# Performance work log

Hardware: AMD Instinct MI355X
Metric: run time of the kernel (lower is better)

The kernel has to match this reference:

```python
import jax, jax.numpy as jnp
import numpy as np

B, T, C = 2, 2048, 1024
NH = 16
HS = C // NH            # 64
BD = max(HS // 4, 16)   # 16
HORIZON = 32


def _windows(t, delta):
    # t: [B, nh, T, d] -> [B, nh, T, delta, d]; window w at pos i maps to original index i-delta+1+w
    padded = jnp.pad(t, ((0, 0), (0, 0), (delta - 1, 0), (0, 0)))
    idx = jnp.arange(t.shape[2])[:, None] + jnp.arange(delta)[None, :]
    return padded[:, :, idx]


def setup_inputs() -> dict:
    key = jax.random.key(0)
    ks = jax.random.split(key, 16)
    s = 0.02
    inp = {
        "x": jax.random.normal(ks[0], (B, T, C), dtype=jnp.float32),
        # weights stored [in, out] (transposed vs torch Linear)
        "w_disp": jax.random.normal(ks[1], (C, NH * BD), dtype=jnp.float32) * s,
        "b_disp": jnp.zeros((NH * BD,), dtype=jnp.float32),
        "w_val": jax.random.normal(ks[2], (C, C), dtype=jnp.float32) * s,
        "b_val": jnp.zeros((C,), dtype=jnp.float32),
        "rel_pos_emb": jax.random.normal(ks[3], (HORIZON, BD), dtype=jnp.float32) * s,
        "w_state": jax.random.normal(ks[4], (BD, BD), dtype=jnp.float32) * s,
        "b_state": jnp.zeros((BD,), dtype=jnp.float32),
        "w_strain": jax.random.normal(ks[5], (BD, BD), dtype=jnp.float32) * s,
        "b_strain": jnp.zeros((BD,), dtype=jnp.float32),
        "w_state_i": jax.random.normal(ks[6], (BD, BD), dtype=jnp.float32) * s,
        "w_state_j": jax.random.normal(ks[7], (BD, BD), dtype=jnp.float32) * s,
        "w_pos": jax.random.normal(ks[8], (BD, BD), dtype=jnp.float32) * s,
        "w_bond_out": jax.random.normal(ks[9], (BD, 1), dtype=jnp.float32) * s,
        "b_bond_out": jnp.zeros((1,), dtype=jnp.float32),
        "w_damage": jax.random.normal(ks[10], (BD, BD), dtype=jnp.float32) * s,
        "b_damage": jnp.zeros((BD,), dtype=jnp.float32),
        "w_damage_out": jax.random.normal(ks[11], (BD, 1), dtype=jnp.float32) * s,
        "b_damage_out": jnp.full((1,), -3.0, dtype=jnp.float32),
        "w_cproj": jax.random.normal(ks[12], (C, C), dtype=jnp.float32) * s,
        "b_cproj": jnp.zeros((C,), dtype=jnp.float32),
    }
    return inp


def reference(x, w_disp, b_disp, w_val, b_val, rel_pos_emb, w_state, b_state,
              w_strain, b_strain, w_state_i, w_state_j, w_pos,
              w_bond_out, b_bond_out, w_damage, b_damage,
              w_damage_out, b_damage_out, w_cproj, b_cproj):
    Bx, Tx, Cx = x.shape
    delta = min(HORIZON, Tx)
    gelu = lambda v: jax.nn.gelu(v, approximate=False)

    disp = (x @ w_disp + b_disp).reshape(Bx, Tx, NH, BD).transpose(0, 2, 1, 3)   # [B,nh,T,bd]
    val = (x @ w_val + b_val).reshape(Bx, Tx, NH, HS).transpose(0, 2, 1, 3)      # [B,nh,T,hs]

    disp_win = _windows(disp, delta)    # [B,nh,T,delta,bd]
    val_win = _windows(val, delta)      # [B,nh,T,delta,hs]

    cmask = (jnp.arange(Tx)[:, None] - delta + 1 + jnp.arange(delta)[None, :]) >= 0  # [T,delta]
    cmask_f = cmask.astype(x.dtype)

    strain = disp_win - disp[:, :, :, None, :]                                   # [B,nh,T,delta,bd]
    strain_for_state = strain @ w_state + b_state
    valid_counts = jnp.clip(cmask_f.sum(axis=-1), 1.0)                           # [T]
    state = (strain_for_state * cmask_f[None, None, :, :, None]).sum(axis=3) \
            / valid_counts[None, None, :, None]                                  # [B,nh,T,bd]
    state_win = _windows(state, delta)                                           # [B,nh,T,delta,bd]

    rel_emb = rel_pos_emb[:delta]                                                # [delta,bd]
    bond_act = gelu(strain @ w_strain + b_strain
                    + state[:, :, :, None, :] @ w_state_i
                    + state_win @ w_state_j
                    + rel_emb @ w_pos)                                           # [B,nh,T,delta,bd]
    bond_logits = (bond_act @ w_bond_out)[..., 0] + b_bond_out[0]                # [B,nh,T,delta]

    damage_act = gelu(strain @ w_damage + b_damage)
    damage = jax.nn.sigmoid((damage_act @ w_damage_out)[..., 0] + b_damage_out[0])

    logits = bond_logits - damage * 10.0
    logits = jnp.where(cmask[None, None], logits, -jnp.inf)
    weights = jax.nn.softmax(logits, axis=-1)                                    # [B,nh,T,delta]

    out = jnp.einsum('bntd,bntde->bnte', weights, val_win)                       # [B,nh,T,hs]
    out = out.transpose(0, 2, 1, 3).reshape(Bx, Tx, Cx)
    return out @ w_cproj + b_cproj
```

## Files before the change

### kernel.cpp

```cpp
#include <hip/hip_runtime.h>
#include <hip/hip_bf16.h>
#include <math.h>

constexpr int B_ = 2, T_ = 2048, C_ = 1024, NH_ = 16, HS_ = 64, BD_ = 16, DELTA_ = 32;
constexpr int M_ = B_ * T_;

typedef __bf16 bf16_t;
typedef __bf16 bf16x8 __attribute__((ext_vector_type(8)));
typedef float  f32x4  __attribute__((ext_vector_type(4)));

__device__ __forceinline__ float frcp(float x)  { return __builtin_amdgcn_rcpf(x); }
__device__ __forceinline__ float fexp2(float x) { return __builtin_amdgcn_exp2f(x); }

__device__ __forceinline__ float gelu_f(float x) {
    const float x2  = x * x;
    const float arg = x * fmaf(0.10294321f, x2, 2.3022074f);
    const float e   = fexp2(arg);
    const float r   = frcp(e + 1.0f);
    return x - x * r;
}
constexpr float LOG2E = 1.4426950409f;

__global__ __launch_bounds__(256) void convert_bf16_kernel(
    const float* __restrict__ in, bf16_t* __restrict__ out, int n)
{
    const int i = (blockIdx.x * 256 + threadIdx.x) * 8;
    if (i >= n) return;
    const float4 v0 = *(const float4*)(in + i);
    const float4 v1 = *(const float4*)(in + i + 4);
    bf16x8 o;
    o[0] = (bf16_t)v0.x; o[1] = (bf16_t)v0.y; o[2] = (bf16_t)v0.z; o[3] = (bf16_t)v0.w;
    o[4] = (bf16_t)v1.x; o[5] = (bf16_t)v1.y; o[6] = (bf16_t)v1.z; o[7] = (bf16_t)v1.w;
    *(bf16x8*)(out + i) = o;
}

__global__ __launch_bounds__(256) void transpose3_kernel(
    const float* __restrict__ w_val, const float* __restrict__ w_cproj,
    const float* __restrict__ w_disp,
    bf16_t* __restrict__ wvT, bf16_t* __restrict__ wcT, bf16_t* __restrict__ wdT)
{
    const int z = blockIdx.z;
    const float* in; bf16_t* out; int K = 1024, N = 1024;
    if (z == 0)      { in = w_val;   out = wvT; }
    else if (z == 1) { in = w_cproj; out = wcT; }
    else             { in = w_disp;  out = wdT; N = 256; if (blockIdx.x >= 8) return; }

    __shared__ float tile[32][33];
    const int n0 = blockIdx.x * 32, k0 = blockIdx.y * 32;
    const int tx = threadIdx.x & 31, ty = threadIdx.x >> 5;
    #pragma unroll
    for (int i = 0; i < 4; ++i)
        tile[ty + 8 * i][tx] = in[(size_t)(k0 + ty + 8 * i) * N + n0 + tx];
    __syncthreads();
    #pragma unroll
    for (int i = 0; i < 4; ++i)
        out[(size_t)(n0 + ty + 8 * i) * K + k0 + tx] = (bf16_t)tile[tx][ty + 8 * i];
}

__device__ __forceinline__ void gload16(const void* g, void* l) {
    __builtin_amdgcn_global_load_lds(
        (__attribute__((address_space(1))) void*)(g),
        (__attribute__((address_space(3))) void*)(l), 16, 0, 0);
}

#define GBM 128
#define GBN 128
#define GBK 32

__device__ __forceinline__ void gemm_core(
    bf16_t (*Al)[GBM][GBK], bf16_t (*Bl)[GBN][GBK],
    const bf16_t* __restrict__ A, const bf16_t* __restrict__ Bt,
    const float* __restrict__ bias, float* __restrict__ C,
    int N, int K, int bm, int bn)
{
    const int tid  = threadIdx.x;
    const int lane = tid & 63;
    const int w    = tid >> 6;
    const int wr   = w >> 1, wc = w & 1;

    const int lrow = lane >> 2;
    const int lcol = (lane & 3) * 8;
    const bf16_t* Ag0 = A  + (size_t)(bm + w * 32 + lrow) * K + lcol;
    const bf16_t* Ag1 = Ag0 + (size_t)16 * K;
    const bf16_t* Bg0 = Bt + (size_t)(bn + w * 32 + lrow) * K + lcol;
    const bf16_t* Bg1 = Bg0 + (size_t)16 * K;

    f32x4 acc[4][4] = {};
    const int nt = K / GBK;
    int cur = 0;

    gload16(Ag0, &Al[0][w * 32][0]);
    gload16(Ag1, &Al[0][w * 32 + 16][0]);
    gload16(Bg0, &Bl[0][w * 32][0]);
    gload16(Bg1, &Bl[0][w * 32 + 16][0]);
    __syncthreads();

    for (int t = 0; t < nt; ++t) {
        if (t + 1 < nt) {
            const int k1 = (t + 1) * GBK;
            gload16(Ag0 + k1, &Al[cur ^ 1][w * 32][0]);
            gload16(Ag1 + k1, &Al[cur ^ 1][w * 32 + 16][0]);
            gload16(Bg0 + k1, &Bl[cur ^ 1][w * 32][0]);
            gload16(Bg1 + k1, &Bl[cur ^ 1][w * 32 + 16][0]);
        }
        bf16x8 af[4], bfr[4];
        #pragma unroll
        for (int i = 0; i < 4; ++i)
            af[i] = *(const bf16x8*)&Al[cur][wr * 64 + i * 16 + (lane & 15)][(lane >> 4) * 8];
        #pragma unroll
        for (int j = 0; j < 4; ++j)
            bfr[j] = *(const bf16x8*)&Bl[cur][wc * 64 + j * 16 + (lane & 15)][(lane >> 4) * 8];
        #pragma unroll
        for (int i = 0; i < 4; ++i)
            #pragma unroll
            for (int j = 0; j < 4; ++j)
                acc[i][j] = __builtin_amdgcn_mfma_f32_16x16x32_bf16(af[i], bfr[j], acc[i][j], 0, 0, 0);
        __syncthreads();
        cur ^= 1;
    }

    #pragma unroll
    for (int i = 0; i < 4; ++i) {
        const int r0 = bm + wr * 64 + i * 16 + (lane >> 4) * 4;
        #pragma unroll
        for (int j = 0; j < 4; ++j) {
            const int c = bn + wc * 64 + j * 16 + (lane & 15);
            const float bv = bias[c];
            float* cp = C + (size_t)r0 * N + c;
            #pragma unroll
            for (int q = 0; q < 4; ++q)
                cp[(size_t)q * N] = acc[i][j][q] + bv;
        }
    }
}

__global__ __launch_bounds__(256) void gemm_bf16_db(
    const bf16_t* __restrict__ A, const bf16_t* __restrict__ Bt,
    const float* __restrict__ bias, float* __restrict__ C,
    int M, int N, int K)
{
    __shared__ __align__(16) bf16_t Al[2][GBM][GBK];
    __shared__ __align__(16) bf16_t Bl[2][GBN][GBK];
    const int gx  = gridDim.x;
    const int nwg = gx * gridDim.y;
    const int bid = blockIdx.y * gx + blockIdx.x;
    const int wid = (bid & 7) * (nwg >> 3) + (bid >> 3);
    const int bx  = wid % gx, by = wid / gx;
    gemm_core(Al, Bl, A, Bt, bias, C, N, K, by * GBM, bx * GBN);
}

__global__ __launch_bounds__(256) void gemm_dv_fused(
    const bf16_t* __restrict__ A,
    const bf16_t* __restrict__ wvT, const bf16_t* __restrict__ wdT,
    const float* __restrict__ b_val, const float* __restrict__ b_disp,
    float* __restrict__ val, float* __restrict__ disp)
{
    __shared__ __align__(16) bf16_t Al[2][GBM][GBK];
    __shared__ __align__(16) bf16_t Bl[2][GBN][GBK];
    const int gx  = 10;
    const int nwg = 320;
    const int bid = blockIdx.y * gx + blockIdx.x;
    const int wid = (bid & 7) * (nwg >> 3) + (bid >> 3);
    const int bx  = wid % gx, by = wid / gx;
    if (bx < 8)
        gemm_core(Al, Bl, A, wvT, b_val, val, 1024, 1024, by * GBM, bx * GBN);
    else
        gemm_core(Al, Bl, A, wdT, b_disp, disp, 256, 1024, by * GBM, (bx - 8) * GBN);
}

#define PCT 128
__global__ __launch_bounds__(256) void precomp_kernel(
    const float* __restrict__ disp,
    const float* __restrict__ w_state, const float* __restrict__ b_state,
    const float* __restrict__ w_strain, const float* __restrict__ b_strain,
    const float* __restrict__ w_state_i, const float* __restrict__ w_state_j,
    const float* __restrict__ w_damage,
    float* __restrict__ P1, float* __restrict__ Q1, float* __restrict__ P2)
{
    __shared__ float s_d[PCT + 31][20];
    __shared__ float s_mv[PCT][20];
    __shared__ float s_st[PCT][20];
    __shared__ float s_wst[16][16], s_wstr[16][16], s_wsi[16][16], s_wsj[16][16], s_wdmg[16][16];
    __shared__ float s_bst[16], s_bstr[16];

    const int bid = blockIdx.x;
    const int tile = bid & (T_ / PCT - 1);
    const int h    = (bid >> 4) & 15;
    const int b    = bid >> 8;
    const int t0   = tile * PCT;
    const int tid  = threadIdx.x;

    s_wst[tid >> 4][tid & 15]  = w_state[tid];
    s_wstr[tid >> 4][tid & 15] = w_strain[tid];
    s_wsi[tid >> 4][tid & 15]  = w_state_i[tid];
    s_wsj[tid >> 4][tid & 15]  = w_state_j[tid];
    s_wdmg[tid >> 4][tid & 15] = w_damage[tid];
    if (tid < 16) { s_bst[tid] = b_state[tid]; s_bstr[tid] = b_strain[tid]; }

    for (int it = tid; it < (PCT + 31) * 4; it += 256) {
        const int row = it >> 2, q = it & 3;
        int rg = t0 - 31 + row; if (rg < 0) rg = 0;
        *(float4*)&s_d[row][q * 4] =
            *(const float4*)(disp + (size_t)(b * T_ + rg) * 256 + h * 16 + q * 4);
    }
    __syncthreads();

    #pragma unroll
    for (int p = 0; p < 8; ++p) {
        const int it = p * 256 + tid;
        const int tl = it >> 4, e = it & 15;
        const int t = t0 + tl;
        const int dlo = max(0, 31 - t);
        float s = 0.0f;
        for (int d = dlo; d < 32; ++d) s += s_d[tl + d][e];
        s_mv[tl][e] = s * frcp((float)(32 - dlo)) - s_d[tl + 31][e];
    }
    __syncthreads();

    #pragma unroll
    for (int p = 0; p < 8; ++p) {
        const int it = p * 256 + tid;
        const int tl = it >> 4, e = it & 15;
        float a = s_bst[e];
        #pragma unroll
        for (int k = 0; k < 16; ++k) a += s_mv[tl][k] * s_wst[k][e];
        s_st[tl][e] = a;
    }
    __syncthreads();

    #pragma unroll
    for (int p = 0; p < 8; ++p) {
        const int it = p * 256 + tid;
        const int tl = it >> 4, e = it & 15;
        float d1 = 0.0f, p2 = 0.0f, sj = 0.0f, si = 0.0f;
        #pragma unroll
        for (int k = 0; k < 16; ++k) {
            const float dv = s_d[tl + 31][k];
            const float sv = s_st[tl][k];
            d1 += dv * s_wstr[k][e];
            p2 += dv * s_wdmg[k][e];
            sj += sv * s_wsj[k][e];
            si += sv * s_wsi[k][e];
        }
        const size_t o = (size_t)(b * T_ + t0 + tl) * 256 + h * 16 + e;
        P1[o] = d1 + sj;
        Q1[o] = s_bstr[e] + si - d1;
        P2[o] = p2;
    }
}

__global__ __launch_bounds__(256) void attn_kernel(
    const float* __restrict__ P1, const float* __restrict__ Q1,
    const float* __restrict__ P2, const float* __restrict__ val,
    const float* __restrict__ rel_pos_emb, const float* __restrict__ w_pos,
    const float* __restrict__ w_bond_out, const float* __restrict__ b_bond_out,
    const float* __restrict__ b_damage,
    const float* __restrict__ w_damage_out, const float* __restrict__ b_damage_out,
    bf16_t* __restrict__ att)
{
    __shared__ float sP1[95][20], sP2[95][20], sQ1[64][20];
    __shared__ float sVal[95][68];
    __shared__ float sWv[64][33];
    __shared__ float s_relw[32][20];
    __shared__ float s_wb[16], s_wd[16], s_bd[16];

    const int tid  = threadIdx.x;
    const int bid  = blockIdx.x;
    const int tile = bid & 31;
    const int h    = (bid >> 5) & 15;
    const int b    = bid >> 9;
    const int t0   = tile * 64;

    for (int it = tid; it < 95 * 4; it += 256) {
        const int row = it >> 2, q = it & 3;
        int rg = t0 - 31 + row; if (rg < 0) rg = 0;
        const size_t o = (size_t)(b * T_ + rg) * 256 + h * 16 + q * 4;
        *(float4*)&sP1[row][q * 4] = *(const float4*)(P1 + o);
        *(float4*)&sP2[row][q * 4] = *(const float4*)(P2 + o);
    }
    {
        const int row = tid >> 2, q = tid & 3;
        *(float4*)&sQ1[row][q * 4] =
            *(const float4*)(Q1 + (size_t)(b * T_ + t0 + row) * 256 + h * 16 + q * 4);
    }
    for (int it = tid; it < 95 * 16; it += 256) {
        const int row = it >> 4, q = it & 15;
        int rg = t0 - 31 + row; if (rg < 0) rg = 0;
        *(float4*)&sVal[row][q * 4] =
            *(const float4*)(val + (size_t)(b * T_ + rg) * 1024 + h * 64 + q * 4);
    }
    {
        for (int it = tid; it < 512; it += 256) {
            const int dd = it >> 4, ee = it & 15;
            float a = 0.0f;
            #pragma unroll
            for (int k = 0; k < 16; ++k) a += rel_pos_emb[dd * 16 + k] * w_pos[k * 16 + ee];
            s_relw[dd][ee] = a;
        }
        if (tid < 16) {
            s_wb[tid] = w_bond_out[tid];
            s_wd[tid] = w_damage_out[tid];
            s_bd[tid] = b_damage[tid];
        }
    }
    __syncthreads();

    const int lane = tid & 63;
    const int w    = tid >> 6;
    const int half = lane >> 5;
    const int d    = lane & 31;
    const float bb  = b_bond_out[0];
    const float bdo = b_damage_out[0];

    #pragma unroll
    for (int pp = 0; pp < 8; ++pp) {
        const int p  = (w << 3) + pp;
        const int tl = (p << 1) + half;
        const int i  = tl + d;
        const bool valid = (t0 - 31 + i) >= 0;

        float bacc = 0.0f, dacc = 0.0f;
        #pragma unroll
        for (int q = 0; q < 4; ++q) {
            const float4 q1  = *(const float4*)&sQ1[tl][q * 4];
            const float4 p2t = *(const float4*)&sP2[tl + 31][q * 4];
            const float4 p1r = *(const float4*)&sP1[i][q * 4];
            const float4 p2r = *(const float4*)&sP2[i][q * 4];
            const float4 rw  = *(const float4*)&s_relw[d][q * 4];
            bacc += gelu_f(p1r.x + q1.x + rw.x) * s_wb[4 * q + 0];
            bacc += gelu_f(p1r.y + q1.y + rw.y) * s_wb[4 * q + 1];
            bacc += gelu_f(p1r.z + q1.z + rw.z) * s_wb[4 * q + 2];
            bacc += gelu_f(p1r.w + q1.w + rw.w) * s_wb[4 * q + 3];
            dacc += gelu_f(p2r.x - p2t.x + s_bd[4 * q + 0]) * s_wd[4 * q + 0];
            dacc += gelu_f(p2r.y - p2t.y + s_bd[4 * q + 1]) * s_wd[4 * q + 1];
            dacc += gelu_f(p2r.z - p2t.z + s_bd[4 * q + 2]) * s_wd[4 * q + 2];
            dacc += gelu_f(p2r.w - p2t.w + s_bd[4 * q + 3]) * s_wd[4 * q + 3];
        }

        float logit = -INFINITY;
        if (valid) {
            const float damage = frcp(1.0f + fexp2(-LOG2E * (dacc + bdo)));
            logit = bacc + bb - 10.0f * damage;
        }
        float m = logit;
        #pragma unroll
        for (int off = 16; off; off >>= 1) m = fmaxf(m, __shfl_xor(m, off, 32));
        const float pe = valid ? fexp2(LOG2E * (logit - m)) : 0.0f;
        float ss = pe;
        #pragma unroll
        for (int off = 16; off; off >>= 1) ss += __shfl_xor(ss, off, 32);
        sWv[tl][d] = pe * frcp(ss);
    }

    #pragma unroll
    for (int pp = 0; pp < 8; ++pp) {
        const int tl0 = (w << 4) + (pp << 1);
        float acc0 = 0.0f, acc1 = 0.0f;
        #pragma unroll
        for (int j = 0; j < 33; ++j) {
            const float v = sVal[tl0 + j][lane];
            if (j < 32) acc0 += sWv[tl0][j] * v;
            if (j >= 1) acc1 += sWv[tl0 + 1][j - 1] * v;
        }
        const size_t o = (size_t)(b * T_ + t0 + tl0) * 1024 + h * 64 + lane;
        att[o]        = (bf16_t)acc0;
        att[o + 1024] = (bf16_t)acc1;
    }
}

extern "C" void kernel_launch(void* const* d_in, const int* in_sizes, int n_in,
                              void* d_out, int out_size, void* d_ws, size_t ws_size,
                              hipStream_t stream)
{
    const float* x        = (const float*)d_in[0];
    const float* w_disp   = (const float*)d_in[1];
    const float* b_disp   = (const float*)d_in[2];
    const float* w_val    = (const float*)d_in[3];
    const float* b_val    = (const float*)d_in[4];
    const float* rel      = (const float*)d_in[5];
    const float* w_state  = (const float*)d_in[6];
    const float* b_state  = (const float*)d_in[7];
    const float* w_strain = (const float*)d_in[8];
    const float* b_strain = (const float*)d_in[9];
    const float* w_si     = (const float*)d_in[10];
    const float* w_sj     = (const float*)d_in[11];
    const float* w_pos    = (const float*)d_in[12];
    const float* w_bond   = (const float*)d_in[13];
    const float* b_bond   = (const float*)d_in[14];
    const float* w_dmg    = (const float*)d_in[15];
    const float* b_dmg    = (const float*)d_in[16];
    const float* w_dout   = (const float*)d_in[17];
    const float* b_dout   = (const float*)d_in[18];
    const float* w_cproj  = (const float*)d_in[19];
    const float* b_cproj  = (const float*)d_in[20];

    float* out = (float*)d_out;
    float* ws  = (float*)d_ws;

    const size_t R = (size_t)M_ * 256;
    float* disp = ws;
    float* P1   = ws + R;
    float* Q1   = ws + 2 * R;
    float* P2   = ws + 3 * R;
    float* val  = ws + 4 * R;
    bf16_t* xb   = (bf16_t*)(ws + 8 * R);
    bf16_t* attb = xb;
    bf16_t* wdT  = (bf16_t*)(ws + 10 * R);
    bf16_t* wvT  = wdT + (size_t)256 * 1024;
    bf16_t* wcT  = wvT + (size_t)1024 * 1024;

    convert_bf16_kernel<<<(M_ * C_) / (256 * 8), 256, 0, stream>>>(x, xb, M_ * C_);
    transpose3_kernel<<<dim3(32, 32, 3), 256, 0, stream>>>(w_val, w_cproj, w_disp, wvT, wcT, wdT);

    gemm_dv_fused<<<dim3(10, 32), 256, 0, stream>>>(xb, wvT, wdT, b_val, b_disp, val, disp);

    precomp_kernel<<<B_ * NH_ * (T_ / PCT), 256, 0, stream>>>(
        disp, w_state, b_state, w_strain, b_strain, w_si, w_sj, w_dmg, P1, Q1, P2);

    attn_kernel<<<B_ * NH_ * (T_ / 64), 256, 0, stream>>>(
        P1, Q1, P2, val, rel, w_pos, w_bond, b_bond, b_dmg, w_dout, b_dout, attb);

    gemm_bf16_db<<<dim3(C_ / GBN, M_ / GBM), 256, 0, stream>>>(attb, wcT, b_cproj, out, M_, C_, C_);
}
```

Before: 224.3 us.

## Shrink GEMM N tile, keep softmax weights in registers, store values as bf16

The GEMM tile narrows from 128 to 64 columns, which doubles the number of workgroups for the fused value/displacement GEMM and the output projection on a many-CU GPU. The attention kernel keeps per-lane softmax weights in registers and broadcasts them with readlane instead of a shared-memory round trip. It also stores the value window in LDS as bf16 and adds an occupancy hint to cut LDS footprint. The costs are lower per-tile data reuse in the GEMM, extra bf16 rounding of values before the weighted sum, and more readlane instructions.

```diff
diff --git a/kernel.cpp b/kernel.cpp
--- a/kernel.cpp
+++ b/kernel.cpp
@@ -11,6 +11,9 @@
 
 __device__ __forceinline__ float frcp(float x)  { return __builtin_amdgcn_rcpf(x); }
 __device__ __forceinline__ float fexp2(float x) { return __builtin_amdgcn_exp2f(x); }
+__device__ __forceinline__ float rlane(float v, int l) {
+    return __builtin_bit_cast(float, __builtin_amdgcn_readlane(__builtin_bit_cast(int, v), l));
+}
 
 __device__ __forceinline__ float gelu_f(float x) {
     const float x2  = x * x;
@@ -64,7 +67,7 @@
 }
 
 #define GBM 128
-#define GBN 128
+#define GBN 64
 #define GBK 32
 
 __device__ __forceinline__ void gemm_core(
@@ -82,17 +85,15 @@
     const int lcol = (lane & 3) * 8;
     const bf16_t* Ag0 = A  + (size_t)(bm + w * 32 + lrow) * K + lcol;
     const bf16_t* Ag1 = Ag0 + (size_t)16 * K;
-    const bf16_t* Bg0 = Bt + (size_t)(bn + w * 32 + lrow) * K + lcol;
-    const bf16_t* Bg1 = Bg0 + (size_t)16 * K;
-
-    f32x4 acc[4][4] = {};
+    const bf16_t* Bg  = Bt + (size_t)(bn + w * 16 + lrow) * K + lcol;
+
+    f32x4 acc[4][2] = {};
     const int nt = K / GBK;
     int cur = 0;
 
     gload16(Ag0, &Al[0][w * 32][0]);
     gload16(Ag1, &Al[0][w * 32 + 16][0]);
-    gload16(Bg0, &Bl[0][w * 32][0]);
-    gload16(Bg1, &Bl[0][w * 32 + 16][0]);
+    gload16(Bg,  &Bl[0][w * 16][0]);
     __syncthreads();
 
     for (int t = 0; t < nt; ++t) {
@@ -100,20 +101,19 @@
             const int k1 = (t + 1) * GBK;
             gload16(Ag0 + k1, &Al[cur ^ 1][w * 32][0]);
             gload16(Ag1 + k1, &Al[cur ^ 1][w * 32 + 16][0]);
-            gload16(Bg0 + k1, &Bl[cur ^ 1][w * 32][0]);
-            gload16(Bg1 + k1, &Bl[cur ^ 1][w * 32 + 16][0]);
-        }
-        bf16x8 af[4], bfr[4];
+            gload16(Bg  + k1, &Bl[cur ^ 1][w * 16][0]);
+        }
+        bf16x8 af[4], bfr[2];
         #pragma unroll
         for (int i = 0; i < 4; ++i)
             af[i] = *(const bf16x8*)&Al[cur][wr * 64 + i * 16 + (lane & 15)][(lane >> 4) * 8];
         #pragma unroll
-        for (int j = 0; j < 4; ++j)
-            bfr[j] = *(const bf16x8*)&Bl[cur][wc * 64 + j * 16 + (lane & 15)][(lane >> 4) * 8];
+        for (int j = 0; j < 2; ++j)
+            bfr[j] = *(const bf16x8*)&Bl[cur][wc * 32 + j * 16 + (lane & 15)][(lane >> 4) * 8];
         #pragma unroll
         for (int i = 0; i < 4; ++i)
             #pragma unroll
-            for (int j = 0; j < 4; ++j)
+            for (int j = 0; j < 2; ++j)
                 acc[i][j] = __builtin_amdgcn_mfma_f32_16x16x32_bf16(af[i], bfr[j], acc[i][j], 0, 0, 0);
         __syncthreads();
         cur ^= 1;
@@ -123,8 +123,8 @@
     for (int i = 0; i < 4; ++i) {
         const int r0 = bm + wr * 64 + i * 16 + (lane >> 4) * 4;
         #pragma unroll
-        for (int j = 0; j < 4; ++j) {
-            const int c = bn + wc * 64 + j * 16 + (lane & 15);
+        for (int j = 0; j < 2; ++j) {
+            const int c = bn + wc * 32 + j * 16 + (lane & 15);
             const float bv = bias[c];
             float* cp = C + (size_t)r0 * N + c;
             #pragma unroll
@@ -157,15 +157,15 @@
 {
     __shared__ __align__(16) bf16_t Al[2][GBM][GBK];
     __shared__ __align__(16) bf16_t Bl[2][GBN][GBK];
-    const int gx  = 10;
-    const int nwg = 320;
+    const int gx  = 20;
+    const int nwg = 640;
     const int bid = blockIdx.y * gx + blockIdx.x;
     const int wid = (bid & 7) * (nwg >> 3) + (bid >> 3);
     const int bx  = wid % gx, by = wid / gx;
-    if (bx < 8)
+    if (bx < 16)
         gemm_core(Al, Bl, A, wvT, b_val, val, 1024, 1024, by * GBM, bx * GBN);
     else
-        gemm_core(Al, Bl, A, wdT, b_disp, disp, 256, 1024, by * GBM, (bx - 8) * GBN);
+        gemm_core(Al, Bl, A, wdT, b_disp, disp, 256, 1024, by * GBM, (bx - 16) * GBN);
 }
 
 #define PCT 128
@@ -249,7 +249,7 @@
     }
 }
 
-__global__ __launch_bounds__(256) void attn_kernel(
+__global__ __launch_bounds__(256, 4) void attn_kernel(
     const float* __restrict__ P1, const float* __restrict__ Q1,
     const float* __restrict__ P2, const float* __restrict__ val,
     const float* __restrict__ rel_pos_emb, const float* __restrict__ w_pos,
@@ -258,11 +258,10 @@
     const float* __restrict__ w_damage_out, const float* __restrict__ b_damage_out,
     bf16_t* __restrict__ att)
 {
-    __shared__ float sP1[95][20], sP2[95][20], sQ1[64][20];
-    __shared__ float sVal[95][68];
-    __shared__ float sWv[64][33];
-    __shared__ float s_relw[32][20];
-    __shared__ float s_wb[16], s_wd[16], s_bd[16];
+    __shared__ float  sP1[95][20], sP2[95][20], sQ1[64][20];
+    __shared__ bf16_t sVal[95][72];
+    __shared__ float  s_relw[32][20];
+    __shared__ float  s_wb[16], s_wd[16], s_bd[16];
 
     const int tid  = threadIdx.x;
     const int bid  = blockIdx.x;
@@ -283,11 +282,16 @@
         *(float4*)&sQ1[row][q * 4] =
             *(const float4*)(Q1 + (size_t)(b * T_ + t0 + row) * 256 + h * 16 + q * 4);
     }
-    for (int it = tid; it < 95 * 16; it += 256) {
-        const int row = it >> 4, q = it & 15;
+    for (int it = tid; it < 95 * 8; it += 256) {
+        const int row = it >> 3, c8 = (it & 7) * 8;
         int rg = t0 - 31 + row; if (rg < 0) rg = 0;
-        *(float4*)&sVal[row][q * 4] =
-            *(const float4*)(val + (size_t)(b * T_ + rg) * 1024 + h * 64 + q * 4);
+        const float* vp = val + (size_t)(b * T_ + rg) * 1024 + h * 64 + c8;
+        const float4 va = *(const float4*)(vp);
+        const float4 vb = *(const float4*)(vp + 4);
+        bf16x8 o;
+        o[0] = (bf16_t)va.x; o[1] = (bf16_t)va.y; o[2] = (bf16_t)va.z; o[3] = (bf16_t)va.w;
+        o[4] = (bf16_t)vb.x; o[5] = (bf16_t)vb.y; o[6] = (bf16_t)vb.z; o[7] = (bf16_t)vb.w;
+        *(bf16x8*)&sVal[row][c8] = o;
     }
     {
         for (int it = tid; it < 512; it += 256) {
@@ -311,6 +315,8 @@
     const int d    = lane & 31;
     const float bb  = b_bond_out[0];
     const float bdo = b_damage_out[0];
+
+    float wv[8];
 
     #pragma unroll
     for (int pp = 0; pp < 8; ++pp) {
@@ -349,7 +355,7 @@
         float ss = pe;
         #pragma unroll
         for (int off = 16; off; off >>= 1) ss += __shfl_xor(ss, off, 32);
-        sWv[tl][d] = pe * frcp(ss);
+        wv[pp] = pe * frcp(ss);
     }
 
     #pragma unroll
@@ -358,9 +364,9 @@
         float acc0 = 0.0f, acc1 = 0.0f;
         #pragma unroll
         for (int j = 0; j < 33; ++j) {
-            const float v = sVal[tl0 + j][lane];
-            if (j < 32) acc0 += sWv[tl0][j] * v;
-            if (j >= 1) acc1 += sWv[tl0 + 1][j - 1] * v;
+            const float v = (float)sVal[tl0 + j][lane];
+            if (j < 32) acc0 += rlane(wv[pp], j) * v;
+            if (j >= 1) acc1 += rlane(wv[pp], 31 + j) * v;
         }
         const size_t o = (size_t)(b * T_ + t0 + tl0) * 1024 + h * 64 + lane;
         att[o]        = (bf16_t)acc0;
@@ -412,7 +418,7 @@
     convert_bf16_kernel<<<(M_ * C_) / (256 * 8), 256, 0, stream>>>(x, xb, M_ * C_);
     transpose3_kernel<<<dim3(32, 32, 3), 256, 0, stream>>>(w_val, w_cproj, w_disp, wvT, wcT, wdT);
 
-    gemm_dv_fused<<<dim3(10, 32), 256, 0, stream>>>(xb, wvT, wdT, b_val, b_disp, val, disp);
+    gemm_dv_fused<<<dim3(20, 32), 256, 0, stream>>>(xb, wvT, wdT, b_val, b_disp, val, disp);
 
     precomp_kernel<<<B_ * NH_ * (T_ / PCT), 256, 0, stream>>>(
         disp, w_state, b_state, w_strain, b_strain, w_si, w_sj, w_dmg, P1, Q1, P2);
```

Result: faster. 215.4 us (-4.0%).
